# Optimization experiments

Measured on AMD Instinct MI355X. Metric: run time of the kernel, lower is better.

Reference implementation:

```python
import jax, jax.numpy as jnp
import numpy as np

NUM_HEADS = 8
HEAD_DIM = 64
HIDDEN = 512
ROPE_THETA = 500000.0


def _make_rope(seq_len, head_dim, theta):
    inv_freq = 1.0 / (theta ** (np.arange(0, head_dim, 2, dtype=np.float32) / head_dim))
    t = np.arange(seq_len, dtype=np.float32)
    freqs = np.outer(t, inv_freq)                  # [S, hd/2]
    emb = np.concatenate([freqs, freqs], axis=-1)  # [S, hd]
    return jnp.asarray(np.cos(emb)), jnp.asarray(np.sin(emb))


def setup_inputs() -> dict:
    key = jax.random.key(0)
    ks = jax.random.split(key, 5)
    B, S, H = 1, 4096, HIDDEN
    num_registers = 32
    hidden_states = jax.random.normal(ks[0], (B, S, H), dtype=jnp.float32)
    scale = 0.02
    Wq = jax.random.normal(ks[1], (H, H), dtype=jnp.float32) * scale
    Wk = jax.random.normal(ks[2], (H, H), dtype=jnp.float32) * scale
    Wv = jax.random.normal(ks[3], (H, H), dtype=jnp.float32) * scale
    Wo = jax.random.normal(ks[4], (H, H), dtype=jnp.float32) * scale
    cos, sin = _make_rope(S - num_registers, HEAD_DIM, ROPE_THETA)
    return {"hidden_states": hidden_states, "Wq": Wq, "Wk": Wk, "Wv": Wv,
            "Wo": Wo, "cos": cos, "sin": sin, "num_registers": num_registers}


def _rotate_half(x):
    x1, x2 = jnp.split(x, 2, axis=-1)
    return jnp.concatenate([-x2, x1], axis=-1)


def _apply_rope(q, k, cos, sin):
    # cos/sin: [S_real, hd] broadcast over [B, H, S_real, hd]
    cos = cos[None, None]
    sin = sin[None, None]
    return q * cos + _rotate_half(q) * sin, k * cos + _rotate_half(k) * sin


def reference(hidden_states, Wq, Wk, Wv, Wo, cos, sin, num_registers):
    B, S, _ = hidden_states.shape
    def proj(W):
        # torch Linear: x @ W.T -> [B, S, H] -> [B, nh, S, hd]
        y = jnp.einsum('bsh,oh->bso', hidden_states, W)
        return y.reshape(B, S, NUM_HEADS, HEAD_DIM).transpose(0, 2, 1, 3)
    q, k, v = proj(Wq), proj(Wk), proj(Wv)

    if num_registers > 0:
        q_reg, q_real = q[:, :, :num_registers], q[:, :, num_registers:]
        k_reg, k_real = k[:, :, :num_registers], k[:, :, num_registers:]
        q_real, k_real = _apply_rope(q_real, k_real, cos, sin)
        q = jnp.concatenate([q_reg, q_real], axis=2)
        k = jnp.concatenate([k_reg, k_real], axis=2)
    else:
        q, k = _apply_rope(q, k, cos, sin)

    scale = 1.0 / jnp.sqrt(jnp.float32(HEAD_DIM))
    scores = jnp.einsum('bhqd,bhkd->bhqk', q, k) * scale  # [B, nh, S, S]
    causal = jnp.tril(jnp.ones((S, S), dtype=bool))
    scores = jnp.where(causal[None, None], scores, jnp.float32(-1e30))
    attn = jax.nn.softmax(scores, axis=-1)
    out = jnp.einsum('bhqk,bhkd->bhqd', attn, v)
    out = out.transpose(0, 2, 1, 3).reshape(B, S, HIDDEN)
    return jnp.einsum('bsh,oh->bso', out, Wo)
```

## Files before the change

### kernel.cpp

```cpp
#include <hip/hip_runtime.h>
#include <cstdint>
#include <cstddef>

#define S_LEN 4096
#define HID   512
#define NHEAD 8
#define HD    64
#define SCALE_LOG2E 0.1803368801111204f

typedef __bf16 bf16;
typedef __bf16 bf16x8 __attribute__((ext_vector_type(8)));
typedef __bf16 bf16x4 __attribute__((ext_vector_type(4)));
typedef float  f32x4  __attribute__((ext_vector_type(4)));

__global__ __launch_bounds__(256) void cvt_in(
    const float* __restrict__ hs, const float* __restrict__ wq,
    const float* __restrict__ wk, const float* __restrict__ wv,
    const float* __restrict__ wo,
    bf16* __restrict__ xb, bf16* __restrict__ wqb, bf16* __restrict__ wkb,
    bf16* __restrict__ wvb, bf16* __restrict__ wob)
{
    int e = (blockIdx.x * 256 + threadIdx.x) * 4;
    const float* s; bf16* d; int o;
    if (e < 2 * 1024 * 1024) { s = hs; d = xb; o = e; }
    else {
        int t = e - 2 * 1024 * 1024;
        int wi = t >> 18;
        o = t & ((1 << 18) - 1);
        s = (wi == 0) ? wq : (wi == 1) ? wk : (wi == 2) ? wv : wo;
        d = (wi == 0) ? wqb : (wi == 1) ? wkb : (wi == 2) ? wvb : wob;
    }
    const float4 v = *(const float4*)(s + o);
    bf16x4 ob;
    ob[0] = (bf16)v.x; ob[1] = (bf16)v.y; ob[2] = (bf16)v.z; ob[3] = (bf16)v.w;
    *(bf16x4*)(d + o) = ob;
}

__global__ __launch_bounds__(256) void gemm_qkv(
    const bf16* __restrict__ Xb,
    const bf16* __restrict__ W0, const bf16* __restrict__ W1, const bf16* __restrict__ W2,
    const float* __restrict__ cosT, const float* __restrict__ sinT,
    const int* __restrict__ nregp,
    bf16* __restrict__ Qh, bf16* __restrict__ Kh, bf16* __restrict__ Vt)
{
    const int z = blockIdx.z;
    const bf16* W = (z == 0) ? W0 : (z == 1 ? W1 : W2);
    const int m0 = blockIdx.y * 64, n0 = blockIdx.x * 128;
    __shared__ bf16 lA[64][8][8];
    __shared__ bf16 lB[128][8][8];
    __shared__ bf16 scratch[64][136];
    const int tid = threadIdx.x;
    const int lane = tid & 63, w = tid >> 6;
    const int l16 = lane & 15, lc = lane >> 4, l7 = lane & 7;
    const int wm = (w & 1) * 32, wn = (w >> 1) * 64;
    f32x4 acc[2][4] = {};

    for (int k0 = 0; k0 < HID; k0 += 64) {
        __syncthreads();
#pragma unroll
        for (int i = 0; i < 2; i++) {
            int uu = tid + 256 * i;
            int m = uu >> 3, c = uu & 7;
            *(bf16x8*)(&lA[m][c ^ (m & 7)][0]) =
                *(const bf16x8*)(Xb + (size_t)(m0 + m) * HID + k0 + 8 * c);
        }
#pragma unroll
        for (int i = 0; i < 4; i++) {
            int uu = tid + 256 * i;
            int m = uu >> 3, c = uu & 7;
            *(bf16x8*)(&lB[m][c ^ (m & 7)][0]) =
                *(const bf16x8*)(W + (size_t)(n0 + m) * HID + k0 + 8 * c);
        }
        __syncthreads();
#pragma unroll
        for (int ks = 0; ks < 2; ks++) {
            bf16x8 af[2], bfr[4];
#pragma unroll
            for (int i = 0; i < 2; i++)
                af[i]  = *(const bf16x8*)(&lA[wm + 16 * i + l16][(4 * ks + lc) ^ l7][0]);
#pragma unroll
            for (int j = 0; j < 4; j++)
                bfr[j] = *(const bf16x8*)(&lB[wn + 16 * j + l16][(4 * ks + lc) ^ l7][0]);
#pragma unroll
            for (int i = 0; i < 2; i++)
#pragma unroll
                for (int j = 0; j < 4; j++)
                    acc[i][j] = __builtin_amdgcn_mfma_f32_16x16x32_bf16(
                        af[i], bfr[j], acc[i][j], 0, 0, 0);
        }
    }

    if (z == 2) {
        const int h = (n0 + wn) >> 6;
#pragma unroll
        for (int i = 0; i < 2; i++) {
            const int s0r = m0 + wm + 16 * i + 4 * lc;
#pragma unroll
            for (int j = 0; j < 4; j++) {
                const int dl = 16 * j + l16;
                bf16x4 o;
#pragma unroll
                for (int r = 0; r < 4; r++) o[r] = (bf16)acc[i][j][r];
                *(bf16x4*)(Vt + ((size_t)(h * HD + dl)) * S_LEN + s0r) = o;
            }
        }
    } else {
        const int nreg = *nregp;
        bf16* dst = (z == 0) ? Qh : Kh;
#pragma unroll
        for (int i = 0; i < 2; i++) {
            const int sl0 = wm + 16 * i + 4 * lc;
#pragma unroll
            for (int r = 0; r < 4; r++) {
                const int s = m0 + sl0 + r;
                float c0 = 1.f, sn0 = 0.f, c1 = 1.f, sn1 = 0.f;
                if (s >= nreg) {
                    const int p = s - nreg;
                    c0  = cosT[(size_t)p * HD + l16];
                    sn0 = sinT[(size_t)p * HD + l16];
                    c1  = cosT[(size_t)p * HD + 16 + l16];
                    sn1 = sinT[(size_t)p * HD + 16 + l16];
                }
                const float x0 = acc[i][0][r], x1 = acc[i][1][r];
                const float x2 = acc[i][2][r], x3 = acc[i][3][r];
                bf16* row = &scratch[sl0 + r][wn];
                row[l16]      = (bf16)(x0 * c0 - x2 * sn0);
                row[l16 + 16] = (bf16)(x1 * c1 - x3 * sn1);
                row[l16 + 32] = (bf16)(x2 * c0 + x0 * sn0);
                row[l16 + 48] = (bf16)(x3 * c1 + x1 * sn1);
            }
        }
        __syncthreads();
        const int h0 = n0 >> 6;
#pragma unroll
        for (int i = 0; i < 4; i++) {
            int u = tid + 256 * i;
            int row = u >> 4, c = u & 15;
            bf16x8 val = *(const bf16x8*)(&scratch[row][c * 8]);
            *(bf16x8*)(dst + ((size_t)(h0 + (c >> 3)) * S_LEN + m0 + row) * HD +
                       (c & 7) * 8) = val;
        }
    }
}

__global__ __launch_bounds__(256) void gemm_out(
    const bf16* __restrict__ X, const bf16* __restrict__ Wb,
    float* __restrict__ Y)
{
    const int m0 = blockIdx.y * 64, n0 = blockIdx.x * 64;
    __shared__ bf16 lA[64][8][8];
    __shared__ bf16 lB[64][8][8];
    const int tid = threadIdx.x;
    const int lane = tid & 63, w = tid >> 6;
    const int l16 = lane & 15, lc = lane >> 4, l7 = lane & 7;
    const int wm = (w & 1) * 32, wn = (w >> 1) * 32;
    f32x4 acc[2][2] = {};

    for (int k0 = 0; k0 < HID; k0 += 64) {
        __syncthreads();
#pragma unroll
        for (int i = 0; i < 2; i++) {
            int uu = tid + 256 * i;
            int m = uu >> 3, c = uu & 7;
            *(bf16x8*)(&lA[m][c ^ (m & 7)][0]) =
                *(const bf16x8*)(X + (size_t)(m0 + m) * HID + k0 + 8 * c);
        }
#pragma unroll
        for (int i = 0; i < 2; i++) {
            int uu = tid + 256 * i;
            int m = uu >> 3, c = uu & 7;
            *(bf16x8*)(&lB[m][c ^ (m & 7)][0]) =
                *(const bf16x8*)(Wb + (size_t)(n0 + m) * HID + k0 + 8 * c);
        }
        __syncthreads();
#pragma unroll
        for (int ks = 0; ks < 2; ks++) {
            bf16x8 af[2], bfr[2];
#pragma unroll
            for (int i = 0; i < 2; i++) {
                af[i]  = *(const bf16x8*)(&lA[wm + 16 * i + l16][(4 * ks + lc) ^ l7][0]);
                bfr[i] = *(const bf16x8*)(&lB[wn + 16 * i + l16][(4 * ks + lc) ^ l7][0]);
            }
#pragma unroll
            for (int i = 0; i < 2; i++)
#pragma unroll
                for (int j = 0; j < 2; j++)
                    acc[i][j] = __builtin_amdgcn_mfma_f32_16x16x32_bf16(
                        af[i], bfr[j], acc[i][j], 0, 0, 0);
        }
    }
#pragma unroll
    for (int i = 0; i < 2; i++) {
        int row = m0 + wm + 16 * i + 4 * lc;
#pragma unroll
        for (int j = 0; j < 2; j++) {
            int col = n0 + wn + 16 * j + l16;
#pragma unroll
            for (int r = 0; r < 4; r++)
                Y[(size_t)(row + r) * HID + col] = acc[i][j][r];
        }
    }
}

__global__ __launch_bounds__(256) void attn_part(
    const bf16* __restrict__ Qh, const bf16* __restrict__ Kh,
    const bf16* __restrict__ Vt, float* __restrict__ Opart,
    float* __restrict__ Lpart)
{
    const int h = blockIdx.x >> 2;
    const int ch = blockIdx.x & 3;
    const int bt = 63 - (int)blockIdx.y;
    const int qb = bt * 64;
    const int nkt = bt + 1;
    const int k0 = (nkt * ch) >> 2;
    const int k1 = (nkt * (ch + 1)) >> 2;
    const int tid = threadIdx.x;
    const int lane = tid & 63, w = tid >> 6;
    const int l16 = lane & 15, lc = lane >> 4, l7 = lane & 7;

    float* Op = Opart + ((size_t)(h * 64 + bt) * 4 + ch) * 4096;
    float* Lp = Lpart + ((size_t)(h * 64 + bt) * 4 + ch) * 64;

    if (k0 >= k1) {
        const f32x4 z = {0.f, 0.f, 0.f, 0.f};
#pragma unroll
        for (int i = 0; i < 4; i++)
            *(f32x4*)(Op + 4 * (tid + 256 * i)) = z;
        if (tid < 64) Lp[tid] = 0.f;
        return;
    }

    __shared__ bf16 lK[64][8][8];
    __shared__ bf16 lV[64][8][8];
    __shared__ bf16 lPT[4][16][76];

    const bf16* Kb_ = Kh + (size_t)h * S_LEN * HD;
    const bf16* Vb_ = Vt + (size_t)h * HD * S_LEN;

    int srow[2], scol[2];
#pragma unroll
    for (int i = 0; i < 2; i++) {
        int uu = tid + 256 * i;
        srow[i] = uu >> 3;
        scol[i] = uu & 7;
    }

    bf16x8 qf[2];
    {
        const bf16* qrow = Qh + (size_t)h * S_LEN * HD + (size_t)(qb + 16 * w + l16) * HD;
        qf[0] = *(const bf16x8*)(qrow + 8 * lc);
        qf[1] = *(const bf16x8*)(qrow + 32 + 8 * lc);
    }
    f32x4 oacc[4] = {};
    float l_sum = 0.f;

    bf16x8 kr[2], vr[2];
#pragma unroll
    for (int i = 0; i < 2; i++) {
        kr[i] = *(const bf16x8*)(Kb_ + (size_t)(k0 * 64 + srow[i]) * HD + 8 * scol[i]);
        vr[i] = *(const bf16x8*)(Vb_ + (size_t)srow[i] * S_LEN + k0 * 64 + 8 * scol[i]);
    }

    for (int kt = k0; kt < k1; kt++) {
#pragma unroll
        for (int i = 0; i < 2; i++) {
            *(bf16x8*)(&lK[srow[i]][scol[i] ^ (srow[i] & 7)][0]) = kr[i];
            *(bf16x8*)(&lV[srow[i]][scol[i] ^ (srow[i] & 7)][0]) = vr[i];
        }
        __syncthreads();

        if (kt + 1 < k1) {
#pragma unroll
            for (int i = 0; i < 2; i++) {
                kr[i] = *(const bf16x8*)(Kb_ + (size_t)((kt + 1) * 64 + srow[i]) * HD +
                                         8 * scol[i]);
                vr[i] = *(const bf16x8*)(Vb_ + (size_t)srow[i] * S_LEN +
                                         (kt + 1) * 64 + 8 * scol[i]);
            }
        }

        f32x4 sacc[4] = {};
#pragma unroll
        for (int ks = 0; ks < 2; ks++)
#pragma unroll
            for (int j = 0; j < 4; j++) {
                bf16x8 kf = *(const bf16x8*)(&lK[16 * j + l16][(4 * ks + lc) ^ l7][0]);
                sacc[j] = __builtin_amdgcn_mfma_f32_16x16x32_bf16(
                    kf, qf[ks], sacc[j], 0, 0, 0);
            }

        float pv[4][4];
#pragma unroll
        for (int j = 0; j < 4; j++)
#pragma unroll
            for (int r = 0; r < 4; r++)
                pv[j][r] = __builtin_amdgcn_exp2f(sacc[j][r] * SCALE_LOG2E);
        if (kt == nkt - 1) {
            const int qg = qb + 16 * w + l16;
#pragma unroll
            for (int j = 0; j < 4; j++)
#pragma unroll
                for (int r = 0; r < 4; r++) {
                    const int keyg = kt * 64 + 16 * j + 4 * lc + r;
                    if (keyg > qg) pv[j][r] = 0.f;
                }
        }
#pragma unroll
        for (int j = 0; j < 4; j++)
            l_sum += (pv[j][0] + pv[j][1]) + (pv[j][2] + pv[j][3]);

#pragma unroll
        for (int j = 0; j < 4; j++) {
            bf16x4 pp;
#pragma unroll
            for (int r = 0; r < 4; r++) pp[r] = (bf16)pv[j][r];
            *(bf16x4*)(&lPT[w][l16][16 * j + 4 * lc]) = pp;
        }
        bf16x8 pb[2];
#pragma unroll
        for (int ks = 0; ks < 2; ks++)
            pb[ks] = *(const bf16x8*)(&lPT[w][l16][32 * ks + 8 * lc]);

#pragma unroll
        for (int ks = 0; ks < 2; ks++)
#pragma unroll
            for (int j = 0; j < 4; j++) {
                bf16x8 vf = *(const bf16x8*)(&lV[16 * j + l16][(4 * ks + lc) ^ l7][0]);
                oacc[j] = __builtin_amdgcn_mfma_f32_16x16x32_bf16(
                    vf, pb[ks], oacc[j], 0, 0, 0);
            }

        __syncthreads();
    }

    l_sum += __shfl_xor(l_sum, 16, 64);
    l_sum += __shfl_xor(l_sum, 32, 64);
    if (lane < 16) Lp[16 * w + l16] = l_sum;

#pragma unroll
    for (int j = 0; j < 4; j++)
        *(f32x4*)(Op + (size_t)(16 * w + l16) * 64 + 16 * j + 4 * lc) = oacc[j];
}

__global__ __launch_bounds__(256) void attn_combine(
    const float* __restrict__ Opart, const float* __restrict__ Lpart,
    bf16* __restrict__ Ob)
{
    const int h = blockIdx.x, bt = blockIdx.y;
    const size_t base = (size_t)(h * 64 + bt) * 4;
    const float* O0 = Opart + base * 4096;
    const float* L0 = Lpart + base * 64;
    const int t = threadIdx.x;
    const int q = t >> 2, dq = (t & 3) * 16;
    const float l = (L0[q] + L0[64 + q]) + (L0[128 + q] + L0[192 + q]);
    const float inv = 1.0f / l;
    bf16* out = Ob + (size_t)(bt * 64 + q) * HID + h * HD + dq;
#pragma unroll
    for (int g = 0; g < 2; g++) {
        bf16x8 o8;
#pragma unroll
        for (int e = 0; e < 2; e++) {
            const int off = q * 64 + dq + 8 * g + 4 * e;
            f32x4 a = *(const f32x4*)(O0 + off);
            f32x4 b = *(const f32x4*)(O0 + 4096 + off);
            f32x4 c = *(const f32x4*)(O0 + 8192 + off);
            f32x4 d = *(const f32x4*)(O0 + 12288 + off);
#pragma unroll
            for (int r = 0; r < 4; r++)
                o8[4 * e + r] = (bf16)(((a[r] + b[r]) + (c[r] + d[r])) * inv);
        }
        *(bf16x8*)(out + 8 * g) = o8;
    }
}

extern "C" void kernel_launch(void* const* d_in, const int* in_sizes, int n_in,
                              void* d_out, int out_size, void* d_ws, size_t ws_size,
                              hipStream_t stream) {
    const float* hs   = (const float*)d_in[0];
    const float* Wq   = (const float*)d_in[1];
    const float* Wk   = (const float*)d_in[2];
    const float* Wv   = (const float*)d_in[3];
    const float* Wo   = (const float*)d_in[4];
    const float* cosT = (const float*)d_in[5];
    const float* sinT = (const float*)d_in[6];
    const int*   nreg = (const int*)d_in[7];

    char* ws = (char*)d_ws;
    const size_t MiB = 1 << 20;
    bf16*  Qh    = (bf16*)(ws);
    bf16*  Kh    = (bf16*)(ws + 4 * MiB);
    bf16*  Vt    = (bf16*)(ws + 8 * MiB);
    bf16*  Ob    = (bf16*)(ws + 12 * MiB);
    float* Opart = (float*)(ws + 16 * MiB);
    float* Lpart = (float*)(ws + 48 * MiB);
    bf16*  Xb    = (bf16*)(ws + 49 * MiB);
    bf16*  Wqb   = (bf16*)(ws + 53 * MiB);
    bf16*  Wkb   = (bf16*)(ws + 53 * MiB + 512 * 1024);
    bf16*  Wvb   = (bf16*)(ws + 54 * MiB);
    bf16*  Wob   = (bf16*)(ws + 54 * MiB + 512 * 1024);

    cvt_in<<<3072, 256, 0, stream>>>(hs, Wq, Wk, Wv, Wo, Xb, Wqb, Wkb, Wvb, Wob);
    gemm_qkv<<<dim3(4, 64, 3), 256, 0, stream>>>(Xb, Wqb, Wkb, Wvb,
                                                 cosT, sinT, nreg, Qh, Kh, Vt);
    attn_part<<<dim3(32, 64), 256, 0, stream>>>(Qh, Kh, Vt, Opart, Lpart);
    attn_combine<<<dim3(8, 64), 256, 0, stream>>>(Opart, Lpart, Ob);
    gemm_out<<<dim3(8, 64), 256, 0, stream>>>(Ob, Wob, (float*)d_out);
}
```

Measured before the change: 135.7 us.

## Make attention blocks single-wave, each processing four query subtiles without barriers

Each attention block now uses one 64-lane wave instead of four waves. The wave loads the K/V tile to shared memory itself and loops over all four 16-row query subtiles. This removes the __syncthreads barriers and reuses the K/V fragments held in registers across subtiles. The cost is the register prefetch of the next K/V tile, much lower thread-level parallelism and higher register pressure.

```diff
diff --git a/kernel.cpp b/kernel.cpp
--- a/kernel.cpp
+++ b/kernel.cpp
@@ -202,7 +202,7 @@
     }
 }
 
-__global__ __launch_bounds__(256) void attn_part(
+__global__ __launch_bounds__(64, 2) void attn_part(
     const bf16* __restrict__ Qh, const bf16* __restrict__ Kh,
     const bf16* __restrict__ Vt, float* __restrict__ Opart,
     float* __restrict__ Lpart)
@@ -214,8 +214,7 @@
     const int nkt = bt + 1;
     const int k0 = (nkt * ch) >> 2;
     const int k1 = (nkt * (ch + 1)) >> 2;
-    const int tid = threadIdx.x;
-    const int lane = tid & 63, w = tid >> 6;
+    const int lane = threadIdx.x;
     const int l16 = lane & 15, lc = lane >> 4, l7 = lane & 7;
 
     float* Op = Opart + ((size_t)(h * 64 + bt) * 4 + ch) * 4096;
@@ -224,122 +223,122 @@
     if (k0 >= k1) {
         const f32x4 z = {0.f, 0.f, 0.f, 0.f};
 #pragma unroll
-        for (int i = 0; i < 4; i++)
-            *(f32x4*)(Op + 4 * (tid + 256 * i)) = z;
-        if (tid < 64) Lp[tid] = 0.f;
+        for (int i = 0; i < 16; i++)
+            *(f32x4*)(Op + 4 * (lane + 64 * i)) = z;
+        Lp[lane] = 0.f;
         return;
     }
 
     __shared__ bf16 lK[64][8][8];
     __shared__ bf16 lV[64][8][8];
-    __shared__ bf16 lPT[4][16][76];
+    __shared__ bf16 lPT[16][76];
 
     const bf16* Kb_ = Kh + (size_t)h * S_LEN * HD;
     const bf16* Vb_ = Vt + (size_t)h * HD * S_LEN;
 
-    int srow[2], scol[2];
-#pragma unroll
-    for (int i = 0; i < 2; i++) {
-        int uu = tid + 256 * i;
-        srow[i] = uu >> 3;
-        scol[i] = uu & 7;
-    }
-
-    bf16x8 qf[2];
-    {
-        const bf16* qrow = Qh + (size_t)h * S_LEN * HD + (size_t)(qb + 16 * w + l16) * HD;
-        qf[0] = *(const bf16x8*)(qrow + 8 * lc);
-        qf[1] = *(const bf16x8*)(qrow + 32 + 8 * lc);
-    }
-    f32x4 oacc[4] = {};
-    float l_sum = 0.f;
-
-    bf16x8 kr[2], vr[2];
-#pragma unroll
-    for (int i = 0; i < 2; i++) {
-        kr[i] = *(const bf16x8*)(Kb_ + (size_t)(k0 * 64 + srow[i]) * HD + 8 * scol[i]);
-        vr[i] = *(const bf16x8*)(Vb_ + (size_t)srow[i] * S_LEN + k0 * 64 + 8 * scol[i]);
-    }
+    bf16x8 qf[4][2];
+#pragma unroll
+    for (int st = 0; st < 4; st++) {
+        const bf16* qrow = Qh + (size_t)h * S_LEN * HD +
+                           (size_t)(qb + st * 16 + l16) * HD;
+        qf[st][0] = *(const bf16x8*)(qrow + 8 * lc);
+        qf[st][1] = *(const bf16x8*)(qrow + 32 + 8 * lc);
+    }
+    f32x4 oacc[4][4] = {};
+    float l_sum[4] = {0.f, 0.f, 0.f, 0.f};
 
     for (int kt = k0; kt < k1; kt++) {
 #pragma unroll
-        for (int i = 0; i < 2; i++) {
-            *(bf16x8*)(&lK[srow[i]][scol[i] ^ (srow[i] & 7)][0]) = kr[i];
-            *(bf16x8*)(&lV[srow[i]][scol[i] ^ (srow[i] & 7)][0]) = vr[i];
-        }
-        __syncthreads();
-
-        if (kt + 1 < k1) {
-#pragma unroll
-            for (int i = 0; i < 2; i++) {
-                kr[i] = *(const bf16x8*)(Kb_ + (size_t)((kt + 1) * 64 + srow[i]) * HD +
-                                         8 * scol[i]);
-                vr[i] = *(const bf16x8*)(Vb_ + (size_t)srow[i] * S_LEN +
-                                         (kt + 1) * 64 + 8 * scol[i]);
-            }
-        }
-
-        f32x4 sacc[4] = {};
+        for (int g = 0; g < 2; g++) {
+            bf16x8 kr[4], vr[4];
+#pragma unroll
+            for (int i = 0; i < 4; i++) {
+                int uu = lane + 64 * (4 * g + i);
+                int rw = uu >> 3, c = uu & 7;
+                kr[i] = *(const bf16x8*)(Kb_ + (size_t)(kt * 64 + rw) * HD + 8 * c);
+                vr[i] = *(const bf16x8*)(Vb_ + (size_t)rw * S_LEN + kt * 64 + 8 * c);
+            }
+#pragma unroll
+            for (int i = 0; i < 4; i++) {
+                int uu = lane + 64 * (4 * g + i);
+                int rw = uu >> 3, c = uu & 7;
+                *(bf16x8*)(&lK[rw][c ^ (rw & 7)][0]) = kr[i];
+                *(bf16x8*)(&lV[rw][c ^ (rw & 7)][0]) = vr[i];
+            }
+        }
+
+        bf16x8 kf[2][4], vf[2][4];
 #pragma unroll
         for (int ks = 0; ks < 2; ks++)
 #pragma unroll
             for (int j = 0; j < 4; j++) {
-                bf16x8 kf = *(const bf16x8*)(&lK[16 * j + l16][(4 * ks + lc) ^ l7][0]);
-                sacc[j] = __builtin_amdgcn_mfma_f32_16x16x32_bf16(
-                    kf, qf[ks], sacc[j], 0, 0, 0);
-            }
-
-        float pv[4][4];
+                kf[ks][j] = *(const bf16x8*)(&lK[16 * j + l16][(4 * ks + lc) ^ l7][0]);
+                vf[ks][j] = *(const bf16x8*)(&lV[16 * j + l16][(4 * ks + lc) ^ l7][0]);
+            }
+
+        const bool diag = (kt == nkt - 1);
+#pragma unroll
+        for (int st = 0; st < 4; st++) {
+            f32x4 sacc[4] = {};
+#pragma unroll
+            for (int ks = 0; ks < 2; ks++)
+#pragma unroll
+                for (int j = 0; j < 4; j++)
+                    sacc[j] = __builtin_amdgcn_mfma_f32_16x16x32_bf16(
+                        kf[ks][j], qf[st][ks], sacc[j], 0, 0, 0);
+
+            float pv[4][4];
+#pragma unroll
+            for (int j = 0; j < 4; j++)
+#pragma unroll
+                for (int r = 0; r < 4; r++)
+                    pv[j][r] = __builtin_amdgcn_exp2f(sacc[j][r] * SCALE_LOG2E);
+            if (diag) {
+                const int qg = qb + st * 16 + l16;
+#pragma unroll
+                for (int j = 0; j < 4; j++)
+#pragma unroll
+                    for (int r = 0; r < 4; r++) {
+                        const int keyg = kt * 64 + 16 * j + 4 * lc + r;
+                        if (keyg > qg) pv[j][r] = 0.f;
+                    }
+            }
+#pragma unroll
+            for (int j = 0; j < 4; j++)
+                l_sum[st] += (pv[j][0] + pv[j][1]) + (pv[j][2] + pv[j][3]);
+
+#pragma unroll
+            for (int j = 0; j < 4; j++) {
+                bf16x4 pp;
+#pragma unroll
+                for (int r = 0; r < 4; r++) pp[r] = (bf16)pv[j][r];
+                *(bf16x4*)(&lPT[l16][16 * j + 4 * lc]) = pp;
+            }
+            bf16x8 pb[2];
+#pragma unroll
+            for (int ks = 0; ks < 2; ks++)
+                pb[ks] = *(const bf16x8*)(&lPT[l16][32 * ks + 8 * lc]);
+
+#pragma unroll
+            for (int ks = 0; ks < 2; ks++)
+#pragma unroll
+                for (int j = 0; j < 4; j++)
+                    oacc[st][j] = __builtin_amdgcn_mfma_f32_16x16x32_bf16(
+                        vf[ks][j], pb[ks], oacc[st][j], 0, 0, 0);
+        }
+    }
+
+#pragma unroll
+    for (int st = 0; st < 4; st++) {
+        float ls = l_sum[st];
+        ls += __shfl_xor(ls, 16, 64);
+        ls += __shfl_xor(ls, 32, 64);
+        if (lane < 16) Lp[st * 16 + l16] = ls;
 #pragma unroll
         for (int j = 0; j < 4; j++)
-#pragma unroll
-            for (int r = 0; r < 4; r++)
-                pv[j][r] = __builtin_amdgcn_exp2f(sacc[j][r] * SCALE_LOG2E);
-        if (kt == nkt - 1) {
-            const int qg = qb + 16 * w + l16;
-#pragma unroll
-            for (int j = 0; j < 4; j++)
-#pragma unroll
-                for (int r = 0; r < 4; r++) {
-                    const int keyg = kt * 64 + 16 * j + 4 * lc + r;
-                    if (keyg > qg) pv[j][r] = 0.f;
-                }
-        }
-#pragma unroll
-        for (int j = 0; j < 4; j++)
-            l_sum += (pv[j][0] + pv[j][1]) + (pv[j][2] + pv[j][3]);
-
-#pragma unroll
-        for (int j = 0; j < 4; j++) {
-            bf16x4 pp;
-#pragma unroll
-            for (int r = 0; r < 4; r++) pp[r] = (bf16)pv[j][r];
-            *(bf16x4*)(&lPT[w][l16][16 * j + 4 * lc]) = pp;
-        }
-        bf16x8 pb[2];
-#pragma unroll
-        for (int ks = 0; ks < 2; ks++)
-            pb[ks] = *(const bf16x8*)(&lPT[w][l16][32 * ks + 8 * lc]);
-
-#pragma unroll
-        for (int ks = 0; ks < 2; ks++)
-#pragma unroll
-            for (int j = 0; j < 4; j++) {
-                bf16x8 vf = *(const bf16x8*)(&lV[16 * j + l16][(4 * ks + lc) ^ l7][0]);
-                oacc[j] = __builtin_amdgcn_mfma_f32_16x16x32_bf16(
-                    vf, pb[ks], oacc[j], 0, 0, 0);
-            }
-
-        __syncthreads();
-    }
-
-    l_sum += __shfl_xor(l_sum, 16, 64);
-    l_sum += __shfl_xor(l_sum, 32, 64);
-    if (lane < 16) Lp[16 * w + l16] = l_sum;
-
-#pragma unroll
-    for (int j = 0; j < 4; j++)
-        *(f32x4*)(Op + (size_t)(16 * w + l16) * 64 + 16 * j + 4 * lc) = oacc[j];
+            *(f32x4*)(Op + (size_t)(st * 16 + l16) * 64 + 16 * j + 4 * lc) =
+                oacc[st][j];
+    }
 }
 
 __global__ __launch_bounds__(256) void attn_combine(
@@ -402,7 +401,7 @@
     cvt_in<<<3072, 256, 0, stream>>>(hs, Wq, Wk, Wv, Wo, Xb, Wqb, Wkb, Wvb, Wob);
     gemm_qkv<<<dim3(4, 64, 3), 256, 0, stream>>>(Xb, Wqb, Wkb, Wvb,
                                                  cosT, sinT, nreg, Qh, Kh, Vt);
-    attn_part<<<dim3(32, 64), 256, 0, stream>>>(Qh, Kh, Vt, Opart, Lpart);
+    attn_part<<<dim3(32, 64), 64, 0, stream>>>(Qh, Kh, Vt, Opart, Lpart);
     attn_combine<<<dim3(8, 64), 256, 0, stream>>>(Opart, Lpart, Ob);
     gemm_out<<<dim3(8, 64), 256, 0, stream>>>(Ob, Wob, (float*)d_out);
 }
```

After: 212.9 us. +56.9%, slower.
